# Performance work log

Hardware: AMD Instinct MI355X
Metric: run time of the kernel (lower is better)

Reference implementation:

```python
import jax, jax.numpy as jnp
import numpy as np

HOP = 768
NCB = 14
DIM = 512
VOCAB = 1024
W_SCALE = 0.02  # keep conv stacks numerically tame


def conv1d(x, w, b, stride=1, padding=0):
    # x: [B,C,L], w: [O,I,K] (torch layout), b: [O]
    y = jax.lax.conv_general_dilated(
        x, w, window_strides=(stride,), padding=[(padding, padding)],
        dimension_numbers=('NCH', 'OIH', 'NCH'))
    return y + b[None, :, None]


def conv_transpose1d(x, w, b, stride, padding):
    # torch ConvTranspose1d weight layout: (in, out, k)
    k = w.shape[2]
    w2 = jnp.flip(jnp.transpose(w, (1, 0, 2)), axis=2)  # -> OIH
    y = jax.lax.conv_general_dilated(
        x, w2, window_strides=(1,),
        padding=[(k - 1 - padding, k - 1 - padding)],
        lhs_dilation=(stride,),
        dimension_numbers=('NCH', 'OIH', 'NCH'))
    return y + b[None, :, None]


def setup_inputs() -> dict:
    key = jax.random.key(0)
    ks = jax.random.split(key, 16)
    f = lambda k, shp, s=W_SCALE: jax.random.normal(k, shp, dtype=jnp.float32) * s
    B, T = 2, 98304  # T = 768 * 128
    return {
        'audio': jax.random.normal(ks[0], (B, 1, T), dtype=jnp.float32),
        'codebooks': jax.random.normal(ks[1], (NCB, VOCAB, DIM), dtype=jnp.float32),
        'ew1': f(ks[2], (256, 1, 7)), 'eb1': f(ks[3], (256,)),
        'ew2': f(ks[4], (512, 256, 5)), 'eb2': f(ks[5], (512,)),
        'ew3': f(ks[6], (NCB * DIM, 512, 3)), 'eb3': f(ks[7], (NCB * DIM,)),
        'dw1': f(ks[8], (NCB * DIM, 512, 5)), 'db1': f(ks[9], (512,)),
        'dw2': f(ks[10], (256, 512, 5)), 'db2': f(ks[11], (256,)),
        'dw3': f(ks[12], (1, 256, 7)), 'db3': f(ks[13], (1,)),
    }


def reference(audio, codebooks, ew1, eb1, ew2, eb2, ew3, eb3,
              dw1, db1, dw2, db2, dw3, db3):
    B = audio.shape[0]
    # ---- encoder ----
    h = jax.nn.relu(conv1d(audio, ew1, eb1, stride=1, padding=3))
    h = jax.nn.relu(conv1d(h, ew2, eb2, stride=HOP, padding=2))
    h = conv1d(h, ew3, eb3, stride=1, padding=1)          # [B, NCB*DIM, S]
    S = h.shape[-1]
    emb = h.reshape(B, NCB, DIM, S).transpose(0, 1, 3, 2)  # [B, NCB, S, DIM]
    # ---- VQ: per-codebook squared L2 distance + argmin (same argmin as cdist) ----
    d2 = (jnp.sum(emb * emb, axis=-1, keepdims=True)            # [B,NCB,S,1]
          - 2.0 * jnp.einsum('bksd,kvd->bksv', emb, codebooks)  # [B,NCB,S,V]
          + jnp.sum(codebooks * codebooks, axis=-1)[None, :, None, :])
    codes = jnp.argmin(d2, axis=-1)                        # [B, NCB, S] int
    # ---- decode: embedding lookup + transposed conv decoder ----
    q = codebooks[jnp.arange(NCB)[None, :, None], codes]   # [B, NCB, S, DIM]
    q = q.transpose(0, 1, 3, 2).reshape(B, NCB * DIM, S)   # [B, NCB*DIM, S]
    a = jax.nn.relu(conv_transpose1d(q, dw1, db1, stride=HOP, padding=2))
    a = jax.nn.relu(conv1d(a, dw2, db2, stride=1, padding=2))
    a = jnp.tanh(conv1d(a, dw3, db3, stride=1, padding=3))
    return a  # [B, 1, (S-1)*HOP + 1]
```

## Files before the change

### kernel.cpp

```cpp
#include <hip/hip_runtime.h>
#include <hip/hip_bf16.h>
#include <math.h>

#define T_IN 98304
#define SS 128
#define NBATCH 2
#define NN 256
#define C1 256
#define C2 512
#define C3 7168
#define NCBK 14
#define DIMV 512
#define VOC 1024
#define TOUT 97537
#define HOP 768

#define OFF_CBN    0L
#define OFF_AB1    14336L
#define OFF_AB2    14848L
#define OFF_CCONST 15104L
#define OFF_H2C    15120L
#define OFF_H2XH   146192L
#define OFF_H2XL   342800L
#define OFF_H3H    539408L
#define OFF_H3L    1456912L
#define OFF_SCORES 2374416L
#define OFF_X1H    2374416L
#define OFF_X1L    2538256L
#define OFF_EW3PH  2374416L
#define OFF_EW3PL  5126928L
#define OFF_DW1T   539408L
#define OFF_XH     539408L
#define OFF_XL     3488528L
#define OFF_CODES  9714448L
#define OFF_QBF    9718032L
#define OFF_A1RAW  10635536L
#define OFF_DW2PH  10635536L
#define OFF_DW2PL  10963216L
#define OFF_A2ACT  11290896L

typedef __attribute__((ext_vector_type(8))) short short8;
typedef __attribute__((ext_vector_type(4))) float f32x4;

static __device__ inline ushort f2bf(float x) {
  __hip_bfloat16 h = __float2bfloat16(x);
  return *reinterpret_cast<ushort*>(&h);
}

static __device__ inline void split8(const float4 x0, const float4 x1,
                                     short8& h, short8& l) {
  float xs[8] = {x0.x, x0.y, x0.z, x0.w, x1.x, x1.y, x1.z, x1.w};
  #pragma unroll
  for (int e = 0; e < 8; ++e) {
    uint b = __float_as_uint(xs[e]);
    h[e] = (short)(b >> 16);
    float r = xs[e] - __uint_as_float(b & 0xffff0000u);
    l[e] = (short)(__float_as_uint(r) >> 16);
  }
}

__global__ void k_cbn(const float* __restrict__ cb, float* __restrict__ cbn) {
  int row = blockIdx.x * 4 + (threadIdx.x >> 6);
  int lane = threadIdx.x & 63;
  const float* p = cb + (long)row * DIMV;
  float s = 0.f;
  for (int d = lane; d < DIMV; d += 64) { float x = p[d]; s += x * x; }
  for (int off = 32; off; off >>= 1) s += __shfl_down(s, off);
  if (lane == 0) cbn[row] = s;
}

__global__ __launch_bounds__(256) void k_prep_ab2(const float* __restrict__ db1,
    const float* __restrict__ dw2, const float* __restrict__ db2,
    float* __restrict__ ab1, float* __restrict__ ab2) {
  __shared__ float red[256];
  int o = blockIdx.x, t = threadIdx.x;
  if (o == 0) { ab1[t] = fmaxf(db1[t], 0.f); ab1[t + 256] = fmaxf(db1[t + 256], 0.f); }
  const float* wp = dw2 + (long)o * C2 * 5;
  float acc = 0.f;
  #pragma unroll
  for (int h = 0; h < 2; ++h) {
    int c = t + h * 256;
    const float* p = wp + c * 5;
    float wsum = p[0] + p[1] + p[2] + p[3] + p[4];
    acc = fmaf(wsum, fmaxf(db1[c], 0.f), acc);
  }
  red[t] = acc;
  __syncthreads();
  for (int off = 128; off; off >>= 1) {
    if (t < off) red[t] += red[t + off];
    __syncthreads();
  }
  if (t == 0) ab2[o] = fmaxf(red[0] + db2[o], 0.f);
}

__global__ __launch_bounds__(256) void k_prep_c(const float* __restrict__ dw3,
    const float* __restrict__ db3, const float* __restrict__ ab2,
    float* __restrict__ cconst) {
  __shared__ float red[256];
  int t = threadIdx.x;
  float wsum3 = 0.f;
  #pragma unroll
  for (int j = 0; j < 7; ++j) wsum3 += dw3[t*7+j];
  red[t] = wsum3 * ab2[t];
  __syncthreads();
  for (int off = 128; off; off >>= 1) {
    if (t < off) red[t] += red[t + off];
    __syncthreads();
  }
  if (t == 0) cconst[0] = tanhf(red[0] + db3[0]);
}

__global__ __launch_bounds__(256) void k_enc1(const float* __restrict__ audio,
    const float* __restrict__ ew1, const float* __restrict__ eb1,
    ushort* __restrict__ X1h, ushort* __restrict__ X1l) {
  int n = blockIdx.x, ic = threadIdx.x;
  int b = n >> 7, s = n & 127;
  const float* ap = audio + (long)b * T_IN;
  int base = HOP * s - 5;
  float a[11];
  #pragma unroll
  for (int w = 0; w < 11; ++w) {
    int ai = base + w;
    a[w] = (ai >= 0 && ai < T_IN) ? ap[ai] : 0.f;
  }
  float w1[7];
  #pragma unroll
  for (int j = 0; j < 7; ++j) w1[j] = ew1[ic*7+j];
  float b1 = eb1[ic];
  long off = (long)n * 1280 + ic * 5;
  #pragma unroll
  for (int jj = 0; jj < 5; ++jj) {
    int tcol = HOP * s + jj - 2;
    float v = 0.f;
    if (tcol >= 0) {
      float acc = b1;
      #pragma unroll
      for (int j = 0; j < 7; ++j) acc = fmaf(w1[j], a[jj + j], acc);
      v = fmaxf(acc, 0.f);
    }
    uint bi = __float_as_uint(v);
    X1h[off + jj] = (ushort)(bi >> 16);
    float r = v - __uint_as_float(bi & 0xffff0000u);
    X1l[off + jj] = (ushort)(__float_as_uint(r) >> 16);
  }
}

__global__ __launch_bounds__(256) void gemm_enc2(const float* __restrict__ ew2,
    const ushort* __restrict__ X1h, const ushort* __restrict__ X1l,
    const float* __restrict__ eb2, float* __restrict__ h2c) {
  __shared__ __align__(16) float red[4 * 2048];
  const int tid = threadIdx.x;
  const int w = tid >> 6, lane = tid & 63;
  const int l15 = lane & 15, quad = lane >> 4;
  const int m0 = blockIdx.x * 32, n0 = blockIdx.y * 64;
  const int kbase = w * 320;
  f32x4 acc[2][4] = {};
  const float*  aB = ew2 + (long)(m0 + l15) * 1280 + kbase + quad * 8;
  const ushort* bhB = X1h + (long)(n0 + l15) * 1280 + kbase + quad * 8;
  const ushort* blB = X1l + (long)(n0 + l15) * 1280 + kbase + quad * 8;
  for (int k0 = 0; k0 < 320; k0 += 32) {
    short8 ah[2], al[2], bh[4], bl[4];
    #pragma unroll
    for (int f = 0; f < 2; ++f) {
      const float* ap = aB + (long)f * 16 * 1280 + k0;
      float4 x0 = *(const float4*)ap;
      float4 x1 = *(const float4*)(ap + 4);
      split8(x0, x1, ah[f], al[f]);
    }
    #pragma unroll
    for (int f = 0; f < 4; ++f) {
      bh[f] = *(const short8*)(bhB + (long)f * 16 * 1280 + k0);
      bl[f] = *(const short8*)(blB + (long)f * 16 * 1280 + k0);
    }
    #pragma unroll
    for (int i = 0; i < 2; ++i)
      #pragma unroll
      for (int j = 0; j < 4; ++j) {
        acc[i][j] = __builtin_amdgcn_mfma_f32_16x16x32_bf16(ah[i], bh[j], acc[i][j], 0, 0, 0);
        acc[i][j] = __builtin_amdgcn_mfma_f32_16x16x32_bf16(ah[i], bl[j], acc[i][j], 0, 0, 0);
        acc[i][j] = __builtin_amdgcn_mfma_f32_16x16x32_bf16(al[i], bh[j], acc[i][j], 0, 0, 0);
      }
  }
  #pragma unroll
  for (int i = 0; i < 2; ++i)
    #pragma unroll
    for (int j = 0; j < 4; ++j)
      *(float4*)&red[w * 2048 + (i * 4 + j) * 256 + lane * 4] = *(float4*)&acc[i][j];
  __syncthreads();
  #pragma unroll
  for (int q = 0; q < 2; ++q) {
    const int c = 2 * w + q;
    const int i = c >> 2, j = c & 3;
    float4 s = make_float4(0.f, 0.f, 0.f, 0.f);
    #pragma unroll
    for (int g = 0; g < 4; ++g) {
      float4 t4 = *(const float4*)&red[g * 2048 + c * 256 + lane * 4];
      s.x += t4.x; s.y += t4.y; s.z += t4.z; s.w += t4.w;
    }
    const int obase = m0 + i * 16 + quad * 4;
    float4 bias = *(const float4*)(eb2 + obase);
    const int n = n0 + j * 16 + l15;
    float4 out;
    out.x = fmaxf(s.x + bias.x, 0.f);
    out.y = fmaxf(s.y + bias.y, 0.f);
    out.z = fmaxf(s.z + bias.z, 0.f);
    out.w = fmaxf(s.w + bias.w, 0.f);
    *(float4*)(h2c + (long)n * C2 + obase) = out;
  }
}

__global__ void k_h2x(const float* __restrict__ h2c, ushort* __restrict__ h2xph,
                      ushort* __restrict__ h2xpl) {
  int idx = blockIdx.x * 256 + threadIdx.x;
  const int total = NN * 1536;
  for (; idx < total; idx += gridDim.x * 256) {
    int grp = idx >> 9;
    int r = idx & 511;
    int e = r & 7, lane = r >> 3;
    int quad = lane >> 4, l15 = lane & 15;
    int nt = grp / 48, kt = grp - nt * 48;
    int n = nt * 16 + l15;
    int k = kt * 32 + quad * 8 + e;
    int ic = k / 3, j = k - ic * 3;
    int s2 = (n & 127) + j - 1;
    int b = n >> 7;
    float v = (s2 >= 0 && s2 < SS) ? h2c[(long)(b*SS + s2)*C2 + ic] : 0.f;
    uint bi = __float_as_uint(v);
    h2xph[idx] = (ushort)(bi >> 16);
    float rr = v - __uint_as_float(bi & 0xffff0000u);
    h2xpl[idx] = (ushort)(__float_as_uint(rr) >> 16);
  }
}

__global__ __launch_bounds__(256) void k_ew3p(const float* __restrict__ ew3,
    ushort* __restrict__ ph, ushort* __restrict__ pl, int mrow0) {
  int o8 = blockIdx.x * 256 + threadIdx.x;
  const int total = 3584 * 1536 / 8;
  if (o8 >= total) return;
  int frag = o8 >> 6, lane = o8 & 63;
  int quad = lane >> 4, l15 = lane & 15;
  int mtL = frag / 48, kt = frag - mtL * 48;
  int m = mrow0 + mtL * 16 + l15;
  int k = kt * 32 + quad * 8;
  const float* s = ew3 + (long)m * 1536 + k;
  float4 x0 = *(const float4*)s;
  float4 x1 = *(const float4*)(s + 4);
  short8 h, l;
  split8(x0, x1, h, l);
  long off = (long)o8 * 8;
  *(short8*)(ph + off) = h;
  *(short8*)(pl + off) = l;
}

__global__ __launch_bounds__(256) void gemm_h3(const ushort* __restrict__ aH,
    const ushort* __restrict__ aL, const ushort* __restrict__ bH,
    const ushort* __restrict__ bL, const float* __restrict__ eb3,
    ushort* __restrict__ h3ph, ushort* __restrict__ h3pl, int mrow0) {
  __shared__ __align__(16) float red[4 * 4096];
  const int tid = threadIdx.x;
  const int w = tid >> 6, lane = tid & 63;
  const int l15 = lane & 15, quad = lane >> 4;
  const int bid = blockIdx.x;
  const int xcd = bid & 7, q = bid >> 3;
  const int mchunk = xcd * 7 + (q >> 2);
  const int nchunk = q & 3;
  const int mtL0 = mchunk * 4, nt0 = nchunk * 4, n0 = nchunk * 64;
  const int kt0 = w * 12;
  f32x4 acc[4][4] = {};
  const ushort* aHB = aH + ((long)(mtL0 * 48 + kt0)) * 512 + lane * 8;
  const ushort* aLB = aL + ((long)(mtL0 * 48 + kt0)) * 512 + lane * 8;
  const ushort* bHB = bH + ((long)(nt0 * 48 + kt0)) * 512 + lane * 8;
  const ushort* bLB = bL + ((long)(nt0 * 48 + kt0)) * 512 + lane * 8;
  for (int kt = 0; kt < 12; ++kt) {
    short8 ah[4], al[4], bh[4], bl[4];
    #pragma unroll
    for (int f = 0; f < 4; ++f) {
      long o = ((long)(f * 48 + kt)) * 512;
      ah[f] = *(const short8*)(aHB + o);
      al[f] = *(const short8*)(aLB + o);
      bh[f] = *(const short8*)(bHB + o);
      bl[f] = *(const short8*)(bLB + o);
    }
    #pragma unroll
    for (int i = 0; i < 4; ++i)
      #pragma unroll
      for (int j = 0; j < 4; ++j) {
        acc[i][j] = __builtin_amdgcn_mfma_f32_16x16x32_bf16(ah[i], bh[j], acc[i][j], 0, 0, 0);
        acc[i][j] = __builtin_amdgcn_mfma_f32_16x16x32_bf16(ah[i], bl[j], acc[i][j], 0, 0, 0);
        acc[i][j] = __builtin_amdgcn_mfma_f32_16x16x32_bf16(al[i], bh[j], acc[i][j], 0, 0, 0);
      }
  }
  #pragma unroll
  for (int i = 0; i < 4; ++i)
    #pragma unroll
    for (int j = 0; j < 4; ++j)
      *(float4*)&red[w * 4096 + (i * 4 + j) * 256 + lane * 4] = *(float4*)&acc[i][j];
  __syncthreads();
  const int mg0 = mrow0 + mchunk * 64 + w * 16 + quad * 4;
  float4 bias = *(const float4*)(eb3 + mg0);
  const int ktS = mg0 >> 5, quadk = (mg0 >> 3) & 3, es = mg0 & 7;
  #pragma unroll
  for (int j = 0; j < 4; ++j) {
    float4 s = *(const float4*)&red[(w * 4 + j) * 256 + lane * 4];
    #pragma unroll
    for (int r = 1; r < 4; ++r) {
      float4 tt = *(const float4*)&red[r * 4096 + (w * 4 + j) * 256 + lane * 4];
      s.x += tt.x; s.y += tt.y; s.z += tt.z; s.w += tt.w;
    }
    const int n = n0 + j * 16 + l15;
    float v0 = s.x + bias.x;
    float v1 = s.y + bias.y;
    float v2 = s.z + bias.z;
    float v3 = s.w + bias.w;
    uint b0 = __float_as_uint(v0), b1 = __float_as_uint(v1);
    uint b2 = __float_as_uint(v2), b3 = __float_as_uint(v3);
    uint2 hp;
    hp.x = (b0 >> 16) | (b1 & 0xffff0000u);
    hp.y = (b2 >> 16) | (b3 & 0xffff0000u);
    float r0 = v0 - __uint_as_float(b0 & 0xffff0000u);
    float r1 = v1 - __uint_as_float(b1 & 0xffff0000u);
    float r2 = v2 - __uint_as_float(b2 & 0xffff0000u);
    float r3 = v3 - __uint_as_float(b3 & 0xffff0000u);
    uint2 lp;
    lp.x = (__float_as_uint(r0) >> 16) | (__float_as_uint(r1) & 0xffff0000u);
    lp.y = (__float_as_uint(r2) >> 16) | (__float_as_uint(r3) & 0xffff0000u);
    long off = ((long)((n >> 4) * 224 + ktS)) * 512 + (quadk * 16 + (n & 15)) * 8 + es;
    *(uint2*)(h3ph + off) = hp;
    *(uint2*)(h3pl + off) = lp;
  }
}

__global__ __launch_bounds__(256) void gemm_scores(const float* __restrict__ cb,
    const ushort* __restrict__ h3ph, const ushort* __restrict__ h3pl,
    const float* __restrict__ cbn, float* __restrict__ scores) {
  __shared__ __align__(16) float red[4 * 4096];
  const int tid = threadIdx.x;
  const int w = tid >> 6, lane = tid & 63;
  const int l15 = lane & 15, quad = lane >> 4;
  const int m0 = blockIdx.x * 64, n0 = blockIdx.y * 64, z = blockIdx.z;
  const int kbase = w * 128;
  f32x4 acc[4][4] = {};
  const float*  aB = cb + (long)z * VOC * DIMV + (long)(m0 + l15) * 512 + kbase + quad * 8;
  const ushort* bHB = h3ph + ((long)((n0 >> 4) * 224 + z * 16 + (kbase >> 5))) * 512 + lane * 8;
  const ushort* bLB = h3pl + ((long)((n0 >> 4) * 224 + z * 16 + (kbase >> 5))) * 512 + lane * 8;
  for (int k0 = 0; k0 < 128; k0 += 32) {
    short8 ah[4], al[4], bh[4], bl[4];
    #pragma unroll
    for (int f = 0; f < 4; ++f) {
      const float* ap = aB + (long)f * 16 * 512 + k0;
      float4 x0 = *(const float4*)ap;
      float4 x1 = *(const float4*)(ap + 4);
      split8(x0, x1, ah[f], al[f]);
      long o = ((long)(f * 224) + (k0 >> 5)) * 512;
      bh[f] = *(const short8*)(bHB + o);
      bl[f] = *(const short8*)(bLB + o);
    }
    #pragma unroll
    for (int i = 0; i < 4; ++i)
      #pragma unroll
      for (int j = 0; j < 4; ++j) {
        acc[i][j] = __builtin_amdgcn_mfma_f32_16x16x32_bf16(ah[i], bh[j], acc[i][j], 0, 0, 0);
        acc[i][j] = __builtin_amdgcn_mfma_f32_16x16x32_bf16(ah[i], bl[j], acc[i][j], 0, 0, 0);
        acc[i][j] = __builtin_amdgcn_mfma_f32_16x16x32_bf16(al[i], bh[j], acc[i][j], 0, 0, 0);
      }
  }
  #pragma unroll
  for (int i = 0; i < 4; ++i)
    #pragma unroll
    for (int j = 0; j < 4; ++j)
      *(float4*)&red[w * 4096 + (i * 4 + j) * 256 + lane * 4] = *(float4*)&acc[i][j];
  __syncthreads();
  const int vbase = m0 + w * 16 + quad * 4;
  float4 cn = *(const float4*)(cbn + z * VOC + vbase);
  #pragma unroll
  for (int j = 0; j < 4; ++j) {
    float4 s = *(const float4*)&red[(w * 4 + j) * 256 + lane * 4];
    #pragma unroll
    for (int r = 1; r < 4; ++r) {
      float4 tt = *(const float4*)&red[r * 4096 + (w * 4 + j) * 256 + lane * 4];
      s.x += tt.x; s.y += tt.y; s.z += tt.z; s.w += tt.w;
    }
    const int n = n0 + j * 16 + l15;
    float4 out;
    out.x = cn.x - 2.f * s.x;
    out.y = cn.y - 2.f * s.y;
    out.z = cn.z - 2.f * s.z;
    out.w = cn.w - 2.f * s.w;
    *(float4*)(scores + ((long)z * NN + n) * VOC + vbase) = out;
  }
}

__global__ void k_argmin(const float* __restrict__ scores, int* __restrict__ codes) {
  int row = blockIdx.x;
  int lane = threadIdx.x;
  const float* p = scores + (long)row * VOC;
  float best = 3.4e38f; int bi = 0;
  for (int i = 0; i < 16; ++i) {
    int v = i * 64 + lane;
    float x = p[v];
    if (x < best) { best = x; bi = v; }
  }
  for (int off = 32; off; off >>= 1) {
    float ob = __shfl_down(best, off);
    int oi = __shfl_down(bi, off);
    if (ob < best || (ob == best && oi < bi)) { best = ob; bi = oi; }
  }
  if (lane == 0) codes[row] = bi;
}

__global__ __launch_bounds__(256) void k_dw1t(const float* __restrict__ dw1,
                                              ushort* __restrict__ dw1p) {
  __shared__ __align__(16) ushort T[64 * 72];
  int t = threadIdx.x;
  int k0 = blockIdx.x * 64, m0 = blockIdx.y * 64;
  int kk = t >> 2, mj = (t & 3) * 16;
  const float* src = dw1 + (long)(k0 + kk) * 2560 + m0 + mj;
  float x[16];
  *(float4*)&x[0]  = *(const float4*)(src);
  *(float4*)&x[4]  = *(const float4*)(src + 4);
  *(float4*)&x[8]  = *(const float4*)(src + 8);
  *(float4*)&x[12] = *(const float4*)(src + 12);
  #pragma unroll
  for (int l = 0; l < 16; ++l)
    T[(mj + l) * 72 + kk] = f2bf(x[l]);
  __syncthreads();
  int mo = t >> 2, kc = (t & 3) * 16;
  const int m = m0 + mo;
  const int mt = m >> 4, l15 = m & 15;
  #pragma unroll
  for (int h = 0; h < 2; ++h) {
    const int kk0 = kc + h * 8;
    const int kglob = k0 + kk0;
    const int kt = kglob >> 5;
    const int quad = (kglob >> 3) & 3;
    uint4 u = *(const uint4*)&T[mo * 72 + kk0];
    *(uint4*)(dw1p + ((long)(mt * 224 + kt)) * 512 + (quad * 16 + l15) * 8) = u;
  }
}

__global__ void k_gather_qbf(const float* __restrict__ cb, const int* __restrict__ codes,
                             ushort* __restrict__ qp) {
  int o = blockIdx.x * 256 + threadIdx.x;
  const int total = NN * C3 / 8;
  if (o >= total) return;
  int frag = o >> 6, r = o & 63;
  int quad = r >> 4, l15 = r & 15;
  int nt = frag / 224, kt = frag - nt * 224;
  int n = nt * 16 + l15;
  int kglob = kt * 32 + quad * 8;
  int kcb = kglob >> 9, d0 = kglob & 511;
  int code = codes[kcb * NN + n];
  const float* s = cb + ((long)(kcb * VOC + code)) * DIMV + d0;
  float4 x0 = *(const float4*)s;
  float4 x1 = *(const float4*)(s + 4);
  uint4 u;
  u.x = (uint)f2bf(x0.x) | ((uint)f2bf(x0.y) << 16);
  u.y = (uint)f2bf(x0.z) | ((uint)f2bf(x0.w) << 16);
  u.z = (uint)f2bf(x1.x) | ((uint)f2bf(x1.y) << 16);
  u.w = (uint)f2bf(x1.z) | ((uint)f2bf(x1.w) << 16);
  ((uint4*)qp)[o] = u;
}

__global__ __launch_bounds__(1024) void gemm_a1_mfma(const ushort* __restrict__ dw1p,
    const ushort* __restrict__ qp, float* __restrict__ a1raw) {
  __shared__ __align__(16) float red[4 * 4096];
  const int tid = threadIdx.x;
  const int w = tid >> 6, lane = tid & 63;
  const int l15 = lane & 15, quad = lane >> 4;
  const int mt0 = blockIdx.x * 4, nt0 = blockIdx.y * 4;
  const int kt0 = w * 14;
  f32x4 acc[4][4] = {};
  const ushort* aB = dw1p + ((long)(mt0 * 224 + kt0)) * 512 + lane * 8;
  const ushort* bB = qp   + ((long)(nt0 * 224 + kt0)) * 512 + lane * 8;
  #pragma unroll 2
  for (int kt = 0; kt < 14; ++kt) {
    short8 ah[4], bh[4];
    #pragma unroll
    for (int f = 0; f < 4; ++f) {
      ah[f] = *(const short8*)(aB + ((long)(f * 224 + kt)) * 512);
      bh[f] = *(const short8*)(bB + ((long)(f * 224 + kt)) * 512);
    }
    #pragma unroll
    for (int i = 0; i < 4; ++i)
      #pragma unroll
      for (int j = 0; j < 4; ++j)
        acc[i][j] = __builtin_amdgcn_mfma_f32_16x16x32_bf16(ah[i], bh[j], acc[i][j], 0, 0, 0);
  }
  float4 rsum = make_float4(0.f, 0.f, 0.f, 0.f);
  #pragma unroll
  for (int r = 0; r < 4; ++r) {
    if ((w >> 2) == r) {
      #pragma unroll
      for (int i = 0; i < 4; ++i)
        #pragma unroll
        for (int j = 0; j < 4; ++j)
          *(float4*)&red[(w & 3) * 4096 + (i * 4 + j) * 256 + lane * 4] = *(float4*)&acc[i][j];
    }
    __syncthreads();
    #pragma unroll
    for (int g = 0; g < 4; ++g) {
      float4 t4 = *(const float4*)&red[g * 4096 + w * 256 + lane * 4];
      rsum.x += t4.x; rsum.y += t4.y; rsum.z += t4.z; rsum.w += t4.w;
    }
    __syncthreads();
  }
  const int ci = w >> 2, cj = w & 3;
  const int n = nt0 * 16 + cj * 16 + l15;
  const int mb = mt0 * 16 + ci * 16 + quad * 4;
  float v[4] = {rsum.x, rsum.y, rsum.z, rsum.w};
  #pragma unroll
  for (int reg = 0; reg < 4; ++reg) {
    int m = mb + reg;
    int c = m / 5, jj = m - c * 5;
    a1raw[((long)(n * 5 + jj)) * C2 + c] = v[reg];
  }
}

__global__ void k_x2(const float* __restrict__ a1raw, const float* __restrict__ ab1g,
                     const float* __restrict__ db1, ushort* __restrict__ Xh,
                     ushort* __restrict__ Xl) {
  int idx = blockIdx.x * 256 + threadIdx.x;
  const int total = 2304 * 2560;
  for (; idx < total; idx += gridDim.x * 256) {
    int grp = idx >> 9;
    int r = idx & 511;
    int e = r & 7, lane = r >> 3;
    int quad = lane >> 4, l15 = lane & 15;
    int nt = grp / 80, kt = grp - nt * 80;
    int nu = nt * 16 + l15;
    int ck = kt * 32 + quad * 8 + e;
    int n = nu / 9, u = nu - n * 9;
    int c = ck / 5, jj = ck - c * 5;
    int w = u + jj;
    int s = n & 127;
    int tc = HOP * s - 6 + w;
    float v;
    if (tc < 0 || tc > TOUT - 1) v = 0.f;
    else if (w >= 4 && w <= 8)
      v = fmaxf(db1[c] + a1raw[((long)(n * 5 + (w - 4))) * C2 + c], 0.f);
    else v = ab1g[c];
    uint bi = __float_as_uint(v);
    Xh[idx] = (ushort)(bi >> 16);
    float rr = v - __uint_as_float(bi & 0xffff0000u);
    Xl[idx] = (ushort)(__float_as_uint(rr) >> 16);
  }
}

__global__ __launch_bounds__(256) void k_dw2p(const float* __restrict__ dw2,
    ushort* __restrict__ ph, ushort* __restrict__ pl) {
  int o8 = blockIdx.x * 256 + threadIdx.x;
  const int total = 256 * 2560 / 8;
  if (o8 >= total) return;
  int frag = o8 >> 6, lane = o8 & 63;
  int quad = lane >> 4, l15 = lane & 15;
  int mt = frag / 80, kt = frag - mt * 80;
  int m = mt * 16 + l15;
  int k = kt * 32 + quad * 8;
  const float* s = dw2 + (long)m * 2560 + k;
  float4 x0 = *(const float4*)s;
  float4 x1 = *(const float4*)(s + 4);
  short8 h, l;
  split8(x0, x1, h, l);
  long off = (long)o8 * 8;
  *(short8*)(ph + off) = h;
  *(short8*)(pl + off) = l;
}

__global__ __launch_bounds__(256) void gemm_dec2(const ushort* __restrict__ aH,
    const ushort* __restrict__ aL, const ushort* __restrict__ bH,
    const ushort* __restrict__ bL, const float* __restrict__ db2,
    float* __restrict__ a2act) {
  __shared__ __align__(16) float red[4 * 4096];
  const int tid = threadIdx.x;
  const int w = tid >> 6, lane = tid & 63;
  const int l15 = lane & 15, quad = lane >> 4;
  const int mt0 = blockIdx.x * 4, nt0 = blockIdx.y * 4;
  const int m0 = mt0 * 16, n0 = nt0 * 16;
  const int kt0 = w * 20;
  f32x4 acc[4][4] = {};
  const ushort* aHB = aH + ((long)(mt0 * 80 + kt0)) * 512 + lane * 8;
  const ushort* aLB = aL + ((long)(mt0 * 80 + kt0)) * 512 + lane * 8;
  const ushort* bHB = bH + ((long)(nt0 * 80 + kt0)) * 512 + lane * 8;
  const ushort* bLB = bL + ((long)(nt0 * 80 + kt0)) * 512 + lane * 8;
  for (int kt = 0; kt < 20; ++kt) {
    short8 ah[4], al[4], bh[4], bl[4];
    #pragma unroll
    for (int f = 0; f < 4; ++f) {
      long o = ((long)(f * 80 + kt)) * 512;
      ah[f] = *(const short8*)(aHB + o);
      al[f] = *(const short8*)(aLB + o);
      bh[f] = *(const short8*)(bHB + o);
      bl[f] = *(const short8*)(bLB + o);
    }
    #pragma unroll
    for (int i = 0; i < 4; ++i)
      #pragma unroll
      for (int j = 0; j < 4; ++j) {
        acc[i][j] = __builtin_amdgcn_mfma_f32_16x16x32_bf16(ah[i], bh[j], acc[i][j], 0, 0, 0);
        acc[i][j] = __builtin_amdgcn_mfma_f32_16x16x32_bf16(ah[i], bl[j], acc[i][j], 0, 0, 0);
        acc[i][j] = __builtin_amdgcn_mfma_f32_16x16x32_bf16(al[i], bh[j], acc[i][j], 0, 0, 0);
      }
  }
  #pragma unroll
  for (int i = 0; i < 4; ++i)
    #pragma unroll
    for (int j = 0; j < 4; ++j)
      *(float4*)&red[w * 4096 + (i * 4 + j) * 256 + lane * 4] = *(float4*)&acc[i][j];
  __syncthreads();
  const int mb = m0 + w * 16 + quad * 4;
  float4 bias = *(const float4*)(db2 + mb);
  #pragma unroll
  for (int j = 0; j < 4; ++j) {
    float4 s = *(const float4*)&red[(w * 4 + j) * 256 + lane * 4];
    #pragma unroll
    for (int r = 1; r < 4; ++r) {
      float4 tt = *(const float4*)&red[r * 4096 + (w * 4 + j) * 256 + lane * 4];
      s.x += tt.x; s.y += tt.y; s.z += tt.z; s.w += tt.w;
    }
    const int nu = n0 + j * 16 + l15;
    float4 out;
    out.x = fmaxf(s.x + bias.x, 0.f);
    out.y = fmaxf(s.y + bias.y, 0.f);
    out.z = fmaxf(s.z + bias.z, 0.f);
    out.w = fmaxf(s.w + bias.w, 0.f);
    *(float4*)(a2act + (long)nu * C1 + mb) = out;
  }
}

__global__ void k_fill(float* __restrict__ outp, const float* __restrict__ cconst) {
  float v = cconst[0];
  int idx = blockIdx.x * 256 + threadIdx.x;
  const int total = NBATCH * TOUT;
  for (; idx < total; idx += gridDim.x * 256) outp[idx] = v;
}

__global__ __launch_bounds__(256) void k_dec3(const float* __restrict__ a2act,
    const float* __restrict__ ab2g, const float* __restrict__ dw3,
    const float* __restrict__ db3, float* __restrict__ outp) {
  __shared__ float sa2[9 * C1];
  __shared__ float sb[C1];
  int n = blockIdx.x;
  int s = n & 127, b = n >> 7;
  int t = threadIdx.x;
  for (int i = t; i < 9 * C1; i += 256) sa2[i] = a2act[(long)n * 9 * C1 + i];
  sb[t] = ab2g[t];
  __syncthreads();
  int wv = t >> 6, lane = t & 63;
  float b3 = db3[0];
  for (int w15 = wv; w15 < 15; w15 += 4) {
    int tc = HOP * s - 7 + w15;
    if (tc < 0 || tc > TOUT - 1) continue;
    float part = 0.f;
    for (int cc = lane; cc < C1; cc += 64) {
      #pragma unroll
      for (int j = 0; j < 7; ++j) {
        int wcol = tc + j - 3;
        float x;
        if (wcol < 0 || wcol > TOUT - 1) x = 0.f;
        else {
          int du = wcol - (HOP * s - 4);
          x = (du >= 0 && du <= 8) ? sa2[du * C1 + cc] : sb[cc];
        }
        part = fmaf(dw3[cc*7+j], x, part);
      }
    }
    for (int off = 32; off; off >>= 1) part += __shfl_down(part, off);
    if (lane == 0) outp[(long)b * TOUT + tc] = tanhf(part + b3);
  }
}

extern "C" void kernel_launch(void* const* d_in, const int* in_sizes, int n_in,
                              void* d_out, int out_size, void* d_ws, size_t ws_size,
                              hipStream_t stream) {
  const float* audio = (const float*)d_in[0];
  const float* cb    = (const float*)d_in[1];
  const float* ew1   = (const float*)d_in[2];
  const float* eb1   = (const float*)d_in[3];
  const float* ew2   = (const float*)d_in[4];
  const float* eb2   = (const float*)d_in[5];
  const float* ew3   = (const float*)d_in[6];
  const float* eb3   = (const float*)d_in[7];
  const float* dw1   = (const float*)d_in[8];
  const float* db1   = (const float*)d_in[9];
  const float* dw2   = (const float*)d_in[10];
  const float* db2   = (const float*)d_in[11];
  const float* dw3   = (const float*)d_in[12];
  const float* db3   = (const float*)d_in[13];
  float* outp = (float*)d_out;
  float* ws = (float*)d_ws;

  float*  cbn    = ws + OFF_CBN;
  float*  ab1    = ws + OFF_AB1;
  float*  ab2    = ws + OFF_AB2;
  float*  cconst = ws + OFF_CCONST;
  float*  h2c    = ws + OFF_H2C;
  ushort* h2xph  = (ushort*)(ws + OFF_H2XH);
  ushort* h2xpl  = (ushort*)(ws + OFF_H2XL);
  ushort* h3ph   = (ushort*)(ws + OFF_H3H);
  ushort* h3pl   = (ushort*)(ws + OFF_H3L);
  float*  scores = ws + OFF_SCORES;
  ushort* X1h    = (ushort*)(ws + OFF_X1H);
  ushort* X1l    = (ushort*)(ws + OFF_X1L);
  ushort* ew3ph  = (ushort*)(ws + OFF_EW3PH);
  ushort* ew3pl  = (ushort*)(ws + OFF_EW3PL);
  ushort* dw1p   = (ushort*)(ws + OFF_DW1T);
  ushort* Xh     = (ushort*)(ws + OFF_XH);
  ushort* Xl     = (ushort*)(ws + OFF_XL);
  int*    codes  = (int*)(ws + OFF_CODES);
  ushort* qp     = (ushort*)(ws + OFF_QBF);
  float*  a1raw  = ws + OFF_A1RAW;
  ushort* dw2ph  = (ushort*)(ws + OFF_DW2PH);
  ushort* dw2pl  = (ushort*)(ws + OFF_DW2PL);
  float*  a2act  = ws + OFF_A2ACT;

  k_cbn<<<3584, 256, 0, stream>>>(cb, cbn);
  k_prep_ab2<<<C1, 256, 0, stream>>>(db1, dw2, db2, ab1, ab2);
  k_prep_c<<<1, 256, 0, stream>>>(dw3, db3, ab2, cconst);
  k_enc1<<<NN, 256, 0, stream>>>(audio, ew1, eb1, X1h, X1l);
  gemm_enc2<<<dim3(16, 4), 256, 0, stream>>>(ew2, X1h, X1l, eb2, h2c);
  k_h2x<<<384, 256, 0, stream>>>(h2c, h2xph, h2xpl);
  k_ew3p<<<2688, 256, 0, stream>>>(ew3, ew3ph, ew3pl, 0);
  gemm_h3<<<224, 256, 0, stream>>>(ew3ph, ew3pl, h2xph, h2xpl, eb3, h3ph, h3pl, 0);
  k_ew3p<<<2688, 256, 0, stream>>>(ew3, ew3ph, ew3pl, 3584);
  gemm_h3<<<224, 256, 0, stream>>>(ew3ph, ew3pl, h2xph, h2xpl, eb3, h3ph, h3pl, 3584);
  gemm_scores<<<dim3(16, 4, 14), 256, 0, stream>>>(cb, h3ph, h3pl, cbn, scores);
  k_argmin<<<NCBK * NN, 64, 0, stream>>>(scores, codes);
  k_dw1t<<<dim3(112, 40), 256, 0, stream>>>(dw1, dw1p);
  k_gather_qbf<<<896, 256, 0, stream>>>(cb, codes, qp);
  gemm_a1_mfma<<<dim3(40, 4), 1024, 0, stream>>>(dw1p, qp, a1raw);
  k_x2<<<4096, 256, 0, stream>>>(a1raw, ab1, db1, Xh, Xl);
  k_dw2p<<<320, 256, 0, stream>>>(dw2, dw2ph, dw2pl);
  gemm_dec2<<<dim3(4, 36), 256, 0, stream>>>(dw2ph, dw2pl, Xh, Xl, db2, a2act);
  k_fill<<<256, 256, 0, stream>>>(outp, cconst);
  k_dec3<<<NN, 256, 0, stream>>>(a2act, ab2, dw3, db3, outp);
}
```

Baseline: 419.0 us.

## Pre-split weights into fragment-packed bf16 pairs and merge h3 GEMM halves

```diff
diff --git a/kernel.cpp b/kernel.cpp
--- a/kernel.cpp
+++ b/kernel.cpp
@@ -27,8 +27,6 @@
 #define OFF_SCORES 2374416L
 #define OFF_X1H    2374416L
 #define OFF_X1L    2538256L
-#define OFF_EW3PH  2374416L
-#define OFF_EW3PL  5126928L
 #define OFF_DW1T   539408L
 #define OFF_XH     539408L
 #define OFF_XL     3488528L
@@ -38,6 +36,12 @@
 #define OFF_DW2PH  10635536L
 #define OFF_DW2PL  10963216L
 #define OFF_A2ACT  11290896L
+#define OFF_CBPH   11880720L
+#define OFF_CBPL   15550736L
+#define OFF_EW3PH  19220752L
+#define OFF_EW3PL  24725776L
+#define OFF_EW2PH  30230800L
+#define OFF_EW2PL  30558480L
 
 typedef __attribute__((ext_vector_type(8))) short short8;
 typedef __attribute__((ext_vector_type(4))) float f32x4;
@@ -69,6 +73,26 @@
   if (lane == 0) cbn[row] = s;
 }
 
+__global__ __launch_bounds__(256) void k_cbp(const float* __restrict__ cb,
+    ushort* __restrict__ ph, ushort* __restrict__ pl) {
+  int o8 = blockIdx.x * 256 + threadIdx.x;
+  const int total = NCBK * VOC * DIMV / 8;
+  if (o8 >= total) return;
+  int frag = o8 >> 6, lane = o8 & 63;
+  int quad = lane >> 4, l15 = lane & 15;
+  int zmt = frag >> 4, kt = frag & 15;
+  int row = zmt * 16 + l15;
+  int k = kt * 32 + quad * 8;
+  const float* s = cb + (long)row * DIMV + k;
+  float4 x0 = *(const float4*)s;
+  float4 x1 = *(const float4*)(s + 4);
+  short8 h, l;
+  split8(x0, x1, h, l);
+  long off = (long)o8 * 8;
+  *(short8*)(ph + off) = h;
+  *(short8*)(pl + off) = l;
+}
+
 __global__ __launch_bounds__(256) void k_prep_ab2(const float* __restrict__ db1,
     const float* __restrict__ dw2, const float* __restrict__ db2,
     float* __restrict__ ab1, float* __restrict__ ab2) {
@@ -127,7 +151,6 @@
   #pragma unroll
   for (int j = 0; j < 7; ++j) w1[j] = ew1[ic*7+j];
   float b1 = eb1[ic];
-  long off = (long)n * 1280 + ic * 5;
   #pragma unroll
   for (int jj = 0; jj < 5; ++jj) {
     int tcol = HOP * s + jj - 2;
@@ -138,39 +161,66 @@
       for (int j = 0; j < 7; ++j) acc = fmaf(w1[j], a[jj + j], acc);
       v = fmaxf(acc, 0.f);
     }
+    int k = ic * 5 + jj;
+    int kt = k >> 5;
+    int lane2 = ((k >> 3) & 3) * 16 + (n & 15);
+    long idx = ((long)((n >> 4) * 40 + kt)) * 512 + lane2 * 8 + (k & 7);
     uint bi = __float_as_uint(v);
-    X1h[off + jj] = (ushort)(bi >> 16);
+    X1h[idx] = (ushort)(bi >> 16);
     float r = v - __uint_as_float(bi & 0xffff0000u);
-    X1l[off + jj] = (ushort)(__float_as_uint(r) >> 16);
-  }
-}
-
-__global__ __launch_bounds__(256) void gemm_enc2(const float* __restrict__ ew2,
-    const ushort* __restrict__ X1h, const ushort* __restrict__ X1l,
-    const float* __restrict__ eb2, float* __restrict__ h2c) {
+    X1l[idx] = (ushort)(__float_as_uint(r) >> 16);
+  }
+}
+
+__global__ __launch_bounds__(256) void k_ew2p(const float* __restrict__ ew2,
+    ushort* __restrict__ ph, ushort* __restrict__ pl) {
+  int o8 = blockIdx.x * 256 + threadIdx.x;
+  const int total = 512 * 1280 / 8;
+  if (o8 >= total) return;
+  int frag = o8 >> 6, lane = o8 & 63;
+  int quad = lane >> 4, l15 = lane & 15;
+  int mt = frag / 40, kt = frag - mt * 40;
+  int m = mt * 16 + l15;
+  int k = kt * 32 + quad * 8;
+  const float* s = ew2 + (long)m * 1280 + k;
+  float4 x0 = *(const float4*)s;
+  float4 x1 = *(const float4*)(s + 4);
+  short8 h, l;
+  split8(x0, x1, h, l);
+  long off = (long)o8 * 8;
+  *(short8*)(ph + off) = h;
+  *(short8*)(pl + off) = l;
+}
+
+__global__ __launch_bounds__(256) void gemm_enc2(const ushort* __restrict__ aH,
+    const ushort* __restrict__ aL, const ushort* __restrict__ bH,
+    const ushort* __restrict__ bL, const float* __restrict__ eb2,
+    float* __restrict__ h2c) {
   __shared__ __align__(16) float red[4 * 2048];
   const int tid = threadIdx.x;
   const int w = tid >> 6, lane = tid & 63;
   const int l15 = lane & 15, quad = lane >> 4;
   const int m0 = blockIdx.x * 32, n0 = blockIdx.y * 64;
-  const int kbase = w * 320;
+  const int mt0 = blockIdx.x * 2, nt0 = blockIdx.y * 4;
+  const int kt0 = w * 10;
   f32x4 acc[2][4] = {};
-  const float*  aB = ew2 + (long)(m0 + l15) * 1280 + kbase + quad * 8;
-  const ushort* bhB = X1h + (long)(n0 + l15) * 1280 + kbase + quad * 8;
-  const ushort* blB = X1l + (long)(n0 + l15) * 1280 + kbase + quad * 8;
-  for (int k0 = 0; k0 < 320; k0 += 32) {
+  const ushort* aHB = aH + ((long)(mt0 * 40 + kt0)) * 512 + lane * 8;
+  const ushort* aLB = aL + ((long)(mt0 * 40 + kt0)) * 512 + lane * 8;
+  const ushort* bHB = bH + ((long)(nt0 * 40 + kt0)) * 512 + lane * 8;
+  const ushort* bLB = bL + ((long)(nt0 * 40 + kt0)) * 512 + lane * 8;
+  for (int kt = 0; kt < 10; ++kt) {
     short8 ah[2], al[2], bh[4], bl[4];
     #pragma unroll
-    for (int f = 0; f < 2; ++f) {
-      const float* ap = aB + (long)f * 16 * 1280 + k0;
-      float4 x0 = *(const float4*)ap;
-      float4 x1 = *(const float4*)(ap + 4);
-      split8(x0, x1, ah[f], al[f]);
+    for (int i = 0; i < 2; ++i) {
+      long o = ((long)(i * 40 + kt)) * 512;
+      ah[i] = *(const short8*)(aHB + o);
+      al[i] = *(const short8*)(aLB + o);
     }
     #pragma unroll
     for (int f = 0; f < 4; ++f) {
-      bh[f] = *(const short8*)(bhB + (long)f * 16 * 1280 + k0);
-      bl[f] = *(const short8*)(blB + (long)f * 16 * 1280 + k0);
+      long o = ((long)(f * 40 + kt)) * 512;
+      bh[f] = *(const short8*)(bHB + o);
+      bl[f] = *(const short8*)(bLB + o);
     }
     #pragma unroll
     for (int i = 0; i < 2; ++i)
@@ -233,14 +283,14 @@
 }
 
 __global__ __launch_bounds__(256) void k_ew3p(const float* __restrict__ ew3,
-    ushort* __restrict__ ph, ushort* __restrict__ pl, int mrow0) {
+    ushort* __restrict__ ph, ushort* __restrict__ pl) {
   int o8 = blockIdx.x * 256 + threadIdx.x;
-  const int total = 3584 * 1536 / 8;
+  const int total = C3 * 1536 / 8;
   if (o8 >= total) return;
   int frag = o8 >> 6, lane = o8 & 63;
   int quad = lane >> 4, l15 = lane & 15;
   int mtL = frag / 48, kt = frag - mtL * 48;
-  int m = mrow0 + mtL * 16 + l15;
+  int m = mtL * 16 + l15;
   int k = kt * 32 + quad * 8;
   const float* s = ew3 + (long)m * 1536 + k;
   float4 x0 = *(const float4*)s;
@@ -255,14 +305,14 @@
 __global__ __launch_bounds__(256) void gemm_h3(const ushort* __restrict__ aH,
     const ushort* __restrict__ aL, const ushort* __restrict__ bH,
     const ushort* __restrict__ bL, const float* __restrict__ eb3,
-    ushort* __restrict__ h3ph, ushort* __restrict__ h3pl, int mrow0) {
+    ushort* __restrict__ h3ph, ushort* __restrict__ h3pl) {
   __shared__ __align__(16) float red[4 * 4096];
   const int tid = threadIdx.x;
   const int w = tid >> 6, lane = tid & 63;
   const int l15 = lane & 15, quad = lane >> 4;
   const int bid = blockIdx.x;
   const int xcd = bid & 7, q = bid >> 3;
-  const int mchunk = xcd * 7 + (q >> 2);
+  const int mchunk = xcd * 14 + (q >> 2);
   const int nchunk = q & 3;
   const int mtL0 = mchunk * 4, nt0 = nchunk * 4, n0 = nchunk * 64;
   const int kt0 = w * 12;
@@ -296,7 +346,7 @@
     for (int j = 0; j < 4; ++j)
       *(float4*)&red[w * 4096 + (i * 4 + j) * 256 + lane * 4] = *(float4*)&acc[i][j];
   __syncthreads();
-  const int mg0 = mrow0 + mchunk * 64 + w * 16 + quad * 4;
+  const int mg0 = mchunk * 64 + w * 16 + quad * 4;
   float4 bias = *(const float4*)(eb3 + mg0);
   const int ktS = mg0 >> 5, quadk = (mg0 >> 3) & 3, es = mg0 & 7;
   #pragma unroll
@@ -330,30 +380,32 @@
   }
 }
 
-__global__ __launch_bounds__(256) void gemm_scores(const float* __restrict__ cb,
-    const ushort* __restrict__ h3ph, const ushort* __restrict__ h3pl,
-    const float* __restrict__ cbn, float* __restrict__ scores) {
+__global__ __launch_bounds__(256) void gemm_scores(const ushort* __restrict__ aH,
+    const ushort* __restrict__ aL, const ushort* __restrict__ bH,
+    const ushort* __restrict__ bL, const float* __restrict__ cbn,
+    float* __restrict__ scores) {
   __shared__ __align__(16) float red[4 * 4096];
   const int tid = threadIdx.x;
   const int w = tid >> 6, lane = tid & 63;
   const int l15 = lane & 15, quad = lane >> 4;
   const int m0 = blockIdx.x * 64, n0 = blockIdx.y * 64, z = blockIdx.z;
-  const int kbase = w * 128;
+  const int mt0 = blockIdx.x * 4;
+  const int kt0 = w * 4;
   f32x4 acc[4][4] = {};
-  const float*  aB = cb + (long)z * VOC * DIMV + (long)(m0 + l15) * 512 + kbase + quad * 8;
-  const ushort* bHB = h3ph + ((long)((n0 >> 4) * 224 + z * 16 + (kbase >> 5))) * 512 + lane * 8;
-  const ushort* bLB = h3pl + ((long)((n0 >> 4) * 224 + z * 16 + (kbase >> 5))) * 512 + lane * 8;
-  for (int k0 = 0; k0 < 128; k0 += 32) {
+  const ushort* aHB = aH + ((long)((z * 64 + mt0) * 16 + kt0)) * 512 + lane * 8;
+  const ushort* aLB = aL + ((long)((z * 64 + mt0) * 16 + kt0)) * 512 + lane * 8;
+  const ushort* bHB = bH + ((long)((n0 >> 4) * 224 + z * 16 + kt0)) * 512 + lane * 8;
+  const ushort* bLB = bL + ((long)((n0 >> 4) * 224 + z * 16 + kt0)) * 512 + lane * 8;
+  for (int kt = 0; kt < 4; ++kt) {
     short8 ah[4], al[4], bh[4], bl[4];
     #pragma unroll
     for (int f = 0; f < 4; ++f) {
-      const float* ap = aB + (long)f * 16 * 512 + k0;
-      float4 x0 = *(const float4*)ap;
-      float4 x1 = *(const float4*)(ap + 4);
-      split8(x0, x1, ah[f], al[f]);
-      long o = ((long)(f * 224) + (k0 >> 5)) * 512;
-      bh[f] = *(const short8*)(bHB + o);
-      bl[f] = *(const short8*)(bLB + o);
+      long oa = ((long)(f * 16 + kt)) * 512;
+      long ob = ((long)(f * 224 + kt)) * 512;
+      ah[f] = *(const short8*)(aHB + oa);
+      al[f] = *(const short8*)(aLB + oa);
+      bh[f] = *(const short8*)(bHB + ob);
+      bl[f] = *(const short8*)(bLB + ob);
     }
     #pragma unroll
     for (int i = 0; i < 4; ++i)
@@ -701,8 +753,12 @@
   float*  scores = ws + OFF_SCORES;
   ushort* X1h    = (ushort*)(ws + OFF_X1H);
   ushort* X1l    = (ushort*)(ws + OFF_X1L);
+  ushort* cbph   = (ushort*)(ws + OFF_CBPH);
+  ushort* cbpl   = (ushort*)(ws + OFF_CBPL);
   ushort* ew3ph  = (ushort*)(ws + OFF_EW3PH);
   ushort* ew3pl  = (ushort*)(ws + OFF_EW3PL);
+  ushort* ew2ph  = (ushort*)(ws + OFF_EW2PH);
+  ushort* ew2pl  = (ushort*)(ws + OFF_EW2PL);
   ushort* dw1p   = (ushort*)(ws + OFF_DW1T);
   ushort* Xh     = (ushort*)(ws + OFF_XH);
   ushort* Xl     = (ushort*)(ws + OFF_XL);
@@ -714,16 +770,16 @@
   float*  a2act  = ws + OFF_A2ACT;
 
   k_cbn<<<3584, 256, 0, stream>>>(cb, cbn);
+  k_cbp<<<3584, 256, 0, stream>>>(cb, cbph, cbpl);
   k_prep_ab2<<<C1, 256, 0, stream>>>(db1, dw2, db2, ab1, ab2);
   k_prep_c<<<1, 256, 0, stream>>>(dw3, db3, ab2, cconst);
   k_enc1<<<NN, 256, 0, stream>>>(audio, ew1, eb1, X1h, X1l);
-  gemm_enc2<<<dim3(16, 4), 256, 0, stream>>>(ew2, X1h, X1l, eb2, h2c);
+  k_ew2p<<<320, 256, 0, stream>>>(ew2, ew2ph, ew2pl);
+  gemm_enc2<<<dim3(16, 4), 256, 0, stream>>>(ew2ph, ew2pl, X1h, X1l, eb2, h2c);
   k_h2x<<<384, 256, 0, stream>>>(h2c, h2xph, h2xpl);
-  k_ew3p<<<2688, 256, 0, stream>>>(ew3, ew3ph, ew3pl, 0);
-  gemm_h3<<<224, 256, 0, stream>>>(ew3ph, ew3pl, h2xph, h2xpl, eb3, h3ph, h3pl, 0);
-  k_ew3p<<<2688, 256, 0, stream>>>(ew3, ew3ph, ew3pl, 3584);
-  gemm_h3<<<224, 256, 0, stream>>>(ew3ph, ew3pl, h2xph, h2xpl, eb3, h3ph, h3pl, 3584);
-  gemm_scores<<<dim3(16, 4, 14), 256, 0, stream>>>(cb, h3ph, h3pl, cbn, scores);
+  k_ew3p<<<5376, 256, 0, stream>>>(ew3, ew3ph, ew3pl);
+  gemm_h3<<<448, 256, 0, stream>>>(ew3ph, ew3pl, h2xph, h2xpl, eb3, h3ph, h3pl);
+  gemm_scores<<<dim3(16, 4, 14), 256, 0, stream>>>(cbph, cbpl, h3ph, h3pl, cbn, scores);
   k_argmin<<<NCBK * NN, 64, 0, stream>>>(scores, codes);
   k_dw1t<<<dim3(112, 40), 256, 0, stream>>>(dw1, dw1p);
   k_gather_qbf<<<896, 256, 0, stream>>>(cb, codes, qp);
```

Measured after the change: 394.1 us. 1.06x faster.
